# Performance work log

Measured on AMD Instinct MI355X. Metric: run time of the kernel, lower is better.

Reference implementation:

```python
import jax, jax.numpy as jnp
import numpy as np

EMB_DIM = 1024
NHEAD = 16
HEAD_DIM = EMB_DIM // NHEAD
SLEN = 1024
BSZ = 8
NEG_INF = -1e30


def setup_inputs() -> dict:
    key = jax.random.key(0)
    ks = jax.random.split(key, 8)
    q = jax.random.normal(ks[0], (SLEN, BSZ, EMB_DIM), dtype=jnp.float32)
    k = jax.random.normal(ks[1], (SLEN, BSZ, EMB_DIM), dtype=jnp.float32)
    v = jax.random.normal(ks[2], (SLEN, BSZ, EMB_DIM), dtype=jnp.float32)
    mask = jax.random.randint(ks[3], (BSZ * NHEAD, SLEN, SLEN), 0, 2).astype(jnp.bool_)
    # xavier_uniform bound for square [E,E] matrices
    bound = float(np.sqrt(6.0 / (EMB_DIM + EMB_DIM)))
    Wq = jax.random.uniform(ks[4], (EMB_DIM, EMB_DIM), jnp.float32, -bound, bound)
    Wk = jax.random.uniform(ks[5], (EMB_DIM, EMB_DIM), jnp.float32, -bound, bound)
    Wv = jax.random.uniform(ks[6], (EMB_DIM, EMB_DIM), jnp.float32, -bound, bound)
    Wo = jax.random.uniform(ks[7], (EMB_DIM, EMB_DIM), jnp.float32, -bound, bound)
    return {"q": q, "k": k, "v": v, "mask": mask, "Wq": Wq, "Wk": Wk, "Wv": Wv, "Wo": Wo}


def reference(q, k, v, mask, Wq, Wk, Wv, Wo):
    slen, bsz, emb = q.shape
    scaling = float(HEAD_DIM) ** -0.5
    # F.linear(x, W) = x @ W.T
    query = q @ Wq.T  # [slen, bsz, E]
    key_ = k @ Wk.T
    value = v @ Wv.T
    # -> [bsz*nhead, slen, head_dim]
    def split_heads(x):
        return x.reshape(slen, bsz * NHEAD, HEAD_DIM).transpose(1, 0, 2)
    query = split_heads(query)
    key_ = split_heads(key_)
    value = split_heads(value)
    attn_weight = jnp.einsum('bqd,bkd->bqk', query, key_) * scaling  # [B*H, S, S]
    attn_weight = jnp.where(mask, NEG_INF, attn_weight)
    attn_score = jax.nn.softmax(attn_weight, axis=-1)
    # attn_mask=True: post-softmax multiplicative mask
    attn_score = attn_score * (~mask).astype(attn_score.dtype)
    # dropout is identity in eval mode
    attn_output = jnp.einsum('bqk,bkd->bqd', attn_score, value)  # [B*H, S, hd]
    attn_output = attn_output.transpose(1, 0, 2).reshape(slen, bsz, emb)
    return attn_output @ Wo.T
```

## Files before the change

### kernel.cpp

```cpp
#include <hip/hip_runtime.h>


typedef __attribute__((ext_vector_type(8))) short bf16x8;
typedef __attribute__((ext_vector_type(8))) unsigned short u16x8;
typedef __attribute__((ext_vector_type(4))) float f32x4;

#define LOG2E 1.44269504088896340736f

__device__ __forceinline__ unsigned short bfbits(float f) {
  unsigned u = __builtin_bit_cast(unsigned, f);
  u += 0x7fffu + ((u >> 16) & 1u);
  return (unsigned short)(u >> 16);
}
__device__ __forceinline__ unsigned pk2(float a, float b) {
  return (unsigned)bfbits(a) | ((unsigned)bfbits(b) << 16);
}
__device__ __forceinline__ void async16(const void* src, void* dst_lds) {
  __builtin_amdgcn_global_load_lds(
      (const __attribute__((address_space(1))) unsigned int*)src,
      (__attribute__((address_space(3))) unsigned int*)dst_lds, 16, 0, 0);
}

__global__ __launch_bounds__(256) void cvt_kernel(
    const float* __restrict__ q, const float* __restrict__ k, const float* __restrict__ v,
    const float* __restrict__ wq, const float* __restrict__ wk,
    const float* __restrict__ wv, const float* __restrict__ wo,
    unsigned short* __restrict__ Xin, unsigned short* __restrict__ Wbf)
{
  const unsigned u = blockIdx.x * 256u + threadIdx.x;
  const float* src;
  unsigned short* dst;
  if (u < 3145728u) {
    const unsigned z = u >> 20, r = u & 1048575u;
    src = (z == 0 ? q : z == 1 ? k : v) + (size_t)r * 8;
    dst = Xin + (size_t)z * 8388608u + (size_t)r * 8;
  } else {
    const unsigned u2 = u - 3145728u, wz = u2 >> 17, r = u2 & 131071u;
    src = (wz == 0 ? wq : wz == 1 ? wk : wz == 2 ? wv : wo) + (size_t)r * 8;
    dst = Wbf + (size_t)wz * 1048576u + (size_t)r * 8;
  }
  f32x4 a = *(const f32x4*)src;
  f32x4 b = *(const f32x4*)(src + 4);
  u16x8 o;
  o[0]=bfbits(a[0]); o[1]=bfbits(a[1]); o[2]=bfbits(a[2]); o[3]=bfbits(a[3]);
  o[4]=bfbits(b[0]); o[5]=bfbits(b[1]); o[6]=bfbits(b[2]); o[7]=bfbits(b[3]);
  *(u16x8*)dst = o;
}

__global__ void detect_mask(const unsigned* __restrict__ m, int* __restrict__ flag)
{
  unsigned ok = 1u;
#pragma unroll 8
  for (int i = 0; i < 64; ++i) {
    unsigned w = m[(threadIdx.x << 6) + i];
    ok &= (w <= 1u) ? 1u : 0u;
  }
  unsigned long long vote = __ballot(ok != 0u);
  if (threadIdx.x == 0) *flag = (vote == ~0ull) ? 1 : 0;
}

template<int OUTF32>
__global__ __launch_bounds__(512) void gemm2ph(
    const unsigned short* __restrict__ A,
    const unsigned short* __restrict__ B,
    void* __restrict__ Cv, float scale, int M, int N, int K)
{
  const int tid = threadIdx.x;
  const int w = tid >> 6, lane = tid & 63, c = lane & 15, g = lane >> 4;
  const int wr = w >> 1, wc = w & 1;

  const int nwg = gridDim.x, cpx = nwg >> 3, bid = blockIdx.x;
  const int swz = (bid & 7) * cpx + (bid >> 3);
  const int ntx = N >> 7;
  const int bx = swz % ntx, by = swz / ntx;
  const int rowA = by * 256, rowB = bx * 128;

  __shared__ unsigned short As[2][256 * 64];
  __shared__ unsigned short Bs[2][128 * 64];

  f32x4 acc[4][4];
#pragma unroll
  for (int i = 0; i < 4; ++i)
#pragma unroll
    for (int j = 0; j < 4; ++j) acc[i][j] = (f32x4){0.f, 0.f, 0.f, 0.f};

  const int srow = tid >> 3, skc = tid & 7;
  const int wbase = (tid & ~63) * 16;

#pragma unroll
  for (int i = 0; i < 4; ++i)
    async16(A + (size_t)(rowA + i * 64 + srow) * K + skc * 8,
            (char*)&As[0][0] + i * 8192 + wbase);
#pragma unroll
  for (int j = 0; j < 2; ++j)
    async16(B + (size_t)(rowB + j * 64 + srow) * K + skc * 8,
            (char*)&Bs[0][0] + j * 8192 + wbase);
  __syncthreads();

  int buf = 0;
  const int nk = K >> 6;
  for (int kt = 0; kt < nk; ++kt) {
    if (kt + 1 < nk) {
      const int k1 = (kt + 1) << 6, bo = buf ^ 1;
#pragma unroll
      for (int i = 0; i < 4; ++i)
        async16(A + (size_t)(rowA + i * 64 + srow) * K + k1 + skc * 8,
                (char*)&As[bo][0] + i * 8192 + wbase);
#pragma unroll
      for (int j = 0; j < 2; ++j)
        async16(B + (size_t)(rowB + j * 64 + srow) * K + k1 + skc * 8,
                (char*)&Bs[bo][0] + j * 8192 + wbase);
    }
    bf16x8 af[4][2], bfr[4][2];
#pragma unroll
    for (int x = 0; x < 4; ++x)
#pragma unroll
      for (int ks = 0; ks < 2; ++ks) {
        af[x][ks]  = *(const bf16x8*)&As[buf][(wr * 64 + x * 16 + c) * 64 + ks * 32 + (g << 3)];
        bfr[x][ks] = *(const bf16x8*)&Bs[buf][(wc * 64 + x * 16 + c) * 64 + ks * 32 + (g << 3)];
      }
#pragma unroll
    for (int ks = 0; ks < 2; ++ks)
#pragma unroll
      for (int mf = 0; mf < 4; ++mf)
#pragma unroll
        for (int nf = 0; nf < 4; ++nf)
          acc[mf][nf] = __builtin_amdgcn_mfma_f32_16x16x32_bf16(af[mf][ks], bfr[nf][ks], acc[mf][nf], 0, 0, 0);
    __syncthreads();
    buf ^= 1;
  }

  const int r0 = rowA + wr * 64, c0 = rowB + wc * 64;
  if (OUTF32) {
    float* O = (float*)Cv;
#pragma unroll
    for (int mf = 0; mf < 4; ++mf)
#pragma unroll
      for (int nf = 0; nf < 4; ++nf)
#pragma unroll
        for (int j = 0; j < 4; ++j)
          O[(size_t)(r0 + mf * 16 + g * 4 + j) * N + c0 + nf * 16 + c] = acc[mf][nf][j] * scale;
  } else {
    unsigned short* O = (unsigned short*)Cv;
#pragma unroll
    for (int mf = 0; mf < 4; ++mf)
#pragma unroll
      for (int nf = 0; nf < 4; ++nf)
#pragma unroll
        for (int j = 0; j < 4; ++j)
          O[(size_t)(r0 + mf * 16 + g * 4 + j) * N + c0 + nf * 16 + c] = bfbits(acc[mf][nf][j] * scale);
  }
}

__global__ __launch_bounds__(256) void transpose_v(
    const unsigned short* __restrict__ Xp2, unsigned short* __restrict__ Vt)
{
  const int tid = threadIdx.x;
  const int bh = blockIdx.y, b = bh >> 4, h = bh & 15;
  const int s0 = blockIdx.x << 6;
  __shared__ unsigned short T[64 * 68];
#pragma unroll
  for (int p = 0; p < 2; ++p) {
    const int idx = (p << 8) + tid, sr = idx >> 3, ch2 = idx & 7;
    *(u16x8*)&T[sr * 68 + ch2 * 8] =
        *(const u16x8*)(Xp2 + ((size_t)((s0 + sr) * 8 + b) << 10) + (h << 6) + ch2 * 8);
  }
  __syncthreads();
#pragma unroll
  for (int p = 0; p < 2; ++p) {
    const int idx = (p << 8) + tid, dr = idx >> 3, ch2 = idx & 7;
    u16x8 o;
#pragma unroll
    for (int e = 0; e < 8; ++e) o[e] = T[(ch2 * 8 + e) * 68 + dr];
    *(u16x8*)(Vt + ((size_t)(bh * 64 + dr) << 10) + s0 + ch2 * 8) = o;
  }
}

__device__ __forceinline__ void load_mask4(unsigned mv[4], const void* maskp, bool mi32,
                                           size_t base, int g) {
  if (mi32) {
    const int* mrow = (const int*)maskp + base + (g << 2);
#pragma unroll
    for (int mf = 0; mf < 4; ++mf) {
      const int4 w4 = *(const int4*)(mrow + mf * 16);
      mv[mf] = (w4.x ? 1u : 0u) | (w4.y ? 0x100u : 0u) | (w4.z ? 0x10000u : 0u) | (w4.w ? 0x1000000u : 0u);
    }
  } else {
    const unsigned char* mrow = (const unsigned char*)maskp + base + (g << 2);
#pragma unroll
    for (int mf = 0; mf < 4; ++mf) mv[mf] = *(const unsigned*)(mrow + mf * 16);
  }
}

__global__ __launch_bounds__(256) void attn_kernel(
    const unsigned short* __restrict__ Qp,
    const unsigned short* __restrict__ Kp,
    const unsigned short* __restrict__ Vt,
    const void*           __restrict__ maskp,
    const int*            __restrict__ mflag,
    unsigned short* __restrict__ AO)
{
  const int tid = threadIdx.x;
  const int w = tid >> 6, lane = tid & 63, c = lane & 15, g = lane >> 4;
  const int bh = blockIdx.y, b = bh >> 4, h = bh & 15;
  const int qb0 = blockIdx.x << 6;
  const int qrow = qb0 + (w << 4) + c;
  const bool mi32 = (*mflag != 0);

  __shared__ unsigned short Ksm[64 * 72];
  __shared__ unsigned short Vsm[64 * 72];
  __shared__ unsigned short Psm[4][16 * 72];

  bf16x8 qf[2];
  {
    const unsigned short* qp = Qp + ((size_t)(qrow * 8 + b) << 10) + (h << 6) + (g << 3);
    qf[0] = *(const bf16x8*)qp;
    qf[1] = *(const bf16x8*)(qp + 32);
  }

  const int row0 = tid >> 3, ch = tid & 7;
  const unsigned short* Vg = Vt + ((size_t)bh << 16);
  const size_t mbase0 = ((size_t)bh << 20) + ((size_t)qrow << 10);

  bf16x8 kr[2], vr[2];
#pragma unroll
  for (int p = 0; p < 2; ++p) {
    const int r = row0 + p * 32;
    kr[p] = *(const bf16x8*)(Kp + ((size_t)(r * 8 + b) << 10) + (h << 6) + (ch << 3));
    vr[p] = *(const bf16x8*)(Vg + ((size_t)r << 10) + (ch << 3));
  }
  unsigned mv[4];
  load_mask4(mv, maskp, mi32, mbase0, g);

  f32x4 oacc[4];
#pragma unroll
  for (int i = 0; i < 4; ++i) oacc[i] = (f32x4){0.f, 0.f, 0.f, 0.f};
  float mrun = -1e30f, lrun = 0.f;

  for (int t = 0; t < 16; ++t) {
    const int kk0 = t << 6;
    __syncthreads();
#pragma unroll
    for (int p = 0; p < 2; ++p) {
      const int r = row0 + p * 32;
      *(bf16x8*)&Ksm[r * 72 + (ch << 3)] = kr[p];
      *(bf16x8*)&Vsm[r * 72 + (ch << 3)] = vr[p];
    }
    __syncthreads();
    unsigned mvN[4];
    if (t < 15) {
      const int kk1 = kk0 + 64;
#pragma unroll
      for (int p = 0; p < 2; ++p) {
        const int r = row0 + p * 32;
        kr[p] = *(const bf16x8*)(Kp + ((size_t)((kk1 + r) * 8 + b) << 10) + (h << 6) + (ch << 3));
        vr[p] = *(const bf16x8*)(Vg + ((size_t)r << 10) + kk1 + (ch << 3));
      }
      load_mask4(mvN, maskp, mi32, mbase0 + kk1, g);
    }
    f32x4 sacc[4];
#pragma unroll
    for (int i = 0; i < 4; ++i) sacc[i] = (f32x4){0.f, 0.f, 0.f, 0.f};
#pragma unroll
    for (int d2 = 0; d2 < 2; ++d2) {
#pragma unroll
      for (int mf = 0; mf < 4; ++mf) {
        bf16x8 kf = *(const bf16x8*)&Ksm[(mf * 16 + c) * 72 + d2 * 32 + (g << 3)];
        sacc[mf] = __builtin_amdgcn_mfma_f32_16x16x32_bf16(kf, qf[d2], sacc[mf], 0, 0, 0);
      }
    }
    float tmax = -1e30f;
#pragma unroll
    for (int mf = 0; mf < 4; ++mf)
#pragma unroll
      for (int j = 0; j < 4; ++j) {
        float s = sacc[mf][j];
        if ((mv[mf] >> (8 * j)) & 0xffu) s = -1e30f;
        sacc[mf][j] = s;
        tmax = fmaxf(tmax, s);
      }
    tmax = fmaxf(tmax, __shfl_xor(tmax, 16));
    tmax = fmaxf(tmax, __shfl_xor(tmax, 32));
    const float mnew = fmaxf(mrun, tmax);
    const float alpha = __builtin_amdgcn_exp2f((mrun - mnew) * LOG2E);
    float tsum = 0.f;
    float pv[4][4];
#pragma unroll
    for (int mf = 0; mf < 4; ++mf)
#pragma unroll
      for (int j = 0; j < 4; ++j) {
        const float p = __builtin_amdgcn_exp2f((sacc[mf][j] - mnew) * LOG2E);
        pv[mf][j] = p;
        tsum += p;
      }
    tsum += __shfl_xor(tsum, 16);
    tsum += __shfl_xor(tsum, 32);
    lrun = lrun * alpha + tsum;
    mrun = mnew;
#pragma unroll
    for (int i = 0; i < 4; ++i) {
      oacc[i][0] *= alpha; oacc[i][1] *= alpha; oacc[i][2] *= alpha; oacc[i][3] *= alpha;
    }
#pragma unroll
    for (int mf = 0; mf < 4; ++mf) {
      uint2 t2;
      t2.x = pk2(pv[mf][0], pv[mf][1]);
      t2.y = pk2(pv[mf][2], pv[mf][3]);
      *(uint2*)&Psm[w][c * 72 + mf * 16 + (g << 2)] = t2;
    }
#pragma unroll
    for (int ks = 0; ks < 2; ++ks) {
      bf16x8 pf = *(const bf16x8*)&Psm[w][c * 72 + ks * 32 + (g << 3)];
#pragma unroll
      for (int mf = 0; mf < 4; ++mf) {
        bf16x8 vf = *(const bf16x8*)&Vsm[(mf * 16 + c) * 72 + ks * 32 + (g << 3)];
        oacc[mf] = __builtin_amdgcn_mfma_f32_16x16x32_bf16(vf, pf, oacc[mf], 0, 0, 0);
      }
    }
    if (t < 15) {
      mv[0] = mvN[0]; mv[1] = mvN[1]; mv[2] = mvN[2]; mv[3] = mvN[3];
    }
  }
  const float inv = 1.0f / lrun;
#pragma unroll
  for (int mf = 0; mf < 4; ++mf) {
    uint2 t2;
    t2.x = pk2(oacc[mf][0] * inv, oacc[mf][1] * inv);
    t2.y = pk2(oacc[mf][2] * inv, oacc[mf][3] * inv);
    *(uint2*)(AO + ((size_t)(qrow * 8 + b) << 10) + (h << 6) + mf * 16 + (g << 2)) = t2;
  }
}

extern "C" void kernel_launch(void* const* d_in, const int* in_sizes, int n_in,
                              void* d_out, int out_size, void* d_ws, size_t ws_size,
                              hipStream_t stream)
{
  const float* q  = (const float*)d_in[0];
  const float* k  = (const float*)d_in[1];
  const float* v  = (const float*)d_in[2];
  const void*  mask = (const void*)d_in[3];
  const float* wq = (const float*)d_in[4];
  const float* wk = (const float*)d_in[5];
  const float* wv = (const float*)d_in[6];
  const float* wo = (const float*)d_in[7];

  unsigned short* ws  = (unsigned short*)d_ws;
  unsigned short* Xin = ws;
  unsigned short* Wbf = ws + 25165824u;
  unsigned short* Xp  = ws + 29360128u;
  unsigned short* Vt  = ws + 8388608u;
  unsigned short* AO  = ws;
  int* mfl            = (int*)(ws + 16777216u);

  cvt_kernel<<<14336, 256, 0, stream>>>(q, k, v, wq, wk, wv, wo, Xin, Wbf);
  gemm2ph<0><<<256, 512, 0, stream>>>(Xin,             Wbf,            Xp,             0.125f, 8192, 1024, 1024);
  gemm2ph<0><<<256, 512, 0, stream>>>(Xin + 8388608u,  Wbf + 1048576u, Xp + 8388608u,  1.0f,   8192, 1024, 1024);
  gemm2ph<0><<<256, 512, 0, stream>>>(Xin + 16777216u, Wbf + 2097152u, Xp + 16777216u, 1.0f,   8192, 1024, 1024);
  detect_mask<<<1, 64, 0, stream>>>((const unsigned*)mask, mfl);
  transpose_v<<<dim3(16, 128), 256, 0, stream>>>(Xp + 16777216u, Vt);
  attn_kernel<<<dim3(16, 128), 256, 0, stream>>>(Xp, Xp + 8388608u, Vt, mask, mfl, AO);
  gemm2ph<1><<<256, 512, 0, stream>>>(AO, Wbf + 3145728u, d_out, 1.0f, 8192, 1024, 1024);
}
```

Before: 311.6 us.

## Pack boolean mask into bitmask inside projection GEMMs and read bits in attention

The three QKV projection GEMM launches now also convert the byte or int mask into a packed 1-bit-per-element buffer, each block handling a slice across its first k-iterations. The attention kernel then reads 64-bit words of mask bits per tile instead of bytes, which cuts mask traffic in the bandwidth-heavy attention pass. The cost is an extra full read of the mask overlapped with GEMM compute, some added GEMM work, and a hardcoded 256-block swizzle. The bf16 conversion store is also reworked to pack pairs of values into 32-bit words.

Result: slower. 346.7 us (+11.2%).

```diff
diff --git a/kernel.cpp b/kernel.cpp
--- a/kernel.cpp
+++ b/kernel.cpp
@@ -19,6 +19,25 @@
   __builtin_amdgcn_global_load_lds(
       (const __attribute__((address_space(1))) unsigned int*)src,
       (__attribute__((address_space(3))) unsigned int*)dst_lds, 16, 0, 0);
+}
+__device__ __forceinline__ unsigned nz4i(uint4 w) {
+  return (w.x ? 1u : 0u) | (w.y ? 2u : 0u) | (w.z ? 4u : 0u) | (w.w ? 8u : 0u);
+}
+__device__ __forceinline__ unsigned nz4b(unsigned w) {
+  return ((w & 0xFFu) ? 1u : 0u) | ((w & 0xFF00u) ? 2u : 0u) |
+         ((w & 0xFF0000u) ? 4u : 0u) | ((w & 0xFF000000u) ? 8u : 0u);
+}
+
+__global__ void detect_mask(const unsigned* __restrict__ m, int* __restrict__ flag)
+{
+  unsigned ok = 1u;
+#pragma unroll 8
+  for (int i = 0; i < 64; ++i) {
+    unsigned w = m[(threadIdx.x << 6) + i];
+    ok &= (w <= 1u) ? 1u : 0u;
+  }
+  unsigned long long vote = __ballot(ok != 0u);
+  if (threadIdx.x == 0) *flag = (vote == ~0ull) ? 1 : 0;
 }
 
 __global__ __launch_bounds__(256) void cvt_kernel(
@@ -41,42 +60,37 @@
   }
   f32x4 a = *(const f32x4*)src;
   f32x4 b = *(const f32x4*)(src + 4);
-  u16x8 o;
-  o[0]=bfbits(a[0]); o[1]=bfbits(a[1]); o[2]=bfbits(a[2]); o[3]=bfbits(a[3]);
-  o[4]=bfbits(b[0]); o[5]=bfbits(b[1]); o[6]=bfbits(b[2]); o[7]=bfbits(b[3]);
-  *(u16x8*)dst = o;
-}
-
-__global__ void detect_mask(const unsigned* __restrict__ m, int* __restrict__ flag)
-{
-  unsigned ok = 1u;
-#pragma unroll 8
-  for (int i = 0; i < 64; ++i) {
-    unsigned w = m[(threadIdx.x << 6) + i];
-    ok &= (w <= 1u) ? 1u : 0u;
-  }
-  unsigned long long vote = __ballot(ok != 0u);
-  if (threadIdx.x == 0) *flag = (vote == ~0ull) ? 1 : 0;
+  uint4 o;
+  o.x = pk2(a[0], a[1]); o.y = pk2(a[2], a[3]);
+  o.z = pk2(b[0], b[1]); o.w = pk2(b[2], b[3]);
+  *(uint4*)dst = o;
 }
 
 template<int OUTF32>
 __global__ __launch_bounds__(512) void gemm2ph(
     const unsigned short* __restrict__ A,
     const unsigned short* __restrict__ B,
-    void* __restrict__ Cv, float scale, int M, int N, int K)
+    void* __restrict__ Cv, float scale, int M, int N, int K,
+    const void* __restrict__ maskp, const int* __restrict__ mflag,
+    unsigned* __restrict__ Mp32, unsigned packLo, unsigned packHi)
 {
   const int tid = threadIdx.x;
   const int w = tid >> 6, lane = tid & 63, c = lane & 15, g = lane >> 4;
   const int wr = w >> 1, wc = w & 1;
 
-  const int nwg = gridDim.x, cpx = nwg >> 3, bid = blockIdx.x;
-  const int swz = (bid & 7) * cpx + (bid >> 3);
+  const int bid = blockIdx.x;
+  const int swz = (bid & 7) * 32 + (bid >> 3);
   const int ntx = N >> 7;
   const int bx = swz % ntx, by = swz / ntx;
   const int rowA = by * 256, rowB = bx * 128;
 
   __shared__ unsigned short As[2][256 * 64];
   __shared__ unsigned short Bs[2][128 * 64];
+
+  const bool doPack = packHi > packLo;
+  const unsigned slice0 = packLo + (unsigned)bid * 5462u;
+  const unsigned slice1 = doPack ? (packHi < slice0 + 5462u ? packHi : slice0 + 5462u) : 0u;
+  const bool mi32 = doPack && (*mflag != 0);
 
   f32x4 acc[4][4];
 #pragma unroll
@@ -111,6 +125,28 @@
         async16(B + (size_t)(rowB + j * 64 + srow) * K + k1 + skc * 8,
                 (char*)&Bs[bo][0] + j * 8192 + wbase);
     }
+    if (doPack && kt < 11) {
+      const unsigned u = slice0 + (unsigned)kt * 512u + tid;
+      if (u < slice1) {
+        unsigned bits = 0u;
+        if (mi32) {
+          const uint4* s = (const uint4*)((const int*)maskp + (size_t)u * 32);
+#pragma unroll
+          for (int hh = 0; hh < 2; ++hh) {
+            const uint4 w0 = s[hh * 4 + 0], w1 = s[hh * 4 + 1];
+            const uint4 w2 = s[hh * 4 + 2], w3 = s[hh * 4 + 3];
+            const unsigned b16 = nz4i(w0) | (nz4i(w1) << 4) | (nz4i(w2) << 8) | (nz4i(w3) << 12);
+            bits |= b16 << (hh * 16);
+          }
+        } else {
+          const uint4* s = (const uint4*)((const unsigned char*)maskp + (size_t)u * 32);
+          const uint4 w0 = s[0], w1 = s[1];
+          bits = nz4b(w0.x) | (nz4b(w0.y) << 4) | (nz4b(w0.z) << 8) | (nz4b(w0.w) << 12) |
+                 (nz4b(w1.x) << 16) | (nz4b(w1.y) << 20) | (nz4b(w1.z) << 24) | (nz4b(w1.w) << 28);
+        }
+        Mp32[u] = bits;
+      }
+    }
     bf16x8 af[4][2], bfr[4][2];
 #pragma unroll
     for (int x = 0; x < 4; ++x)
@@ -176,28 +212,11 @@
   }
 }
 
-__device__ __forceinline__ void load_mask4(unsigned mv[4], const void* maskp, bool mi32,
-                                           size_t base, int g) {
-  if (mi32) {
-    const int* mrow = (const int*)maskp + base + (g << 2);
-#pragma unroll
-    for (int mf = 0; mf < 4; ++mf) {
-      const int4 w4 = *(const int4*)(mrow + mf * 16);
-      mv[mf] = (w4.x ? 1u : 0u) | (w4.y ? 0x100u : 0u) | (w4.z ? 0x10000u : 0u) | (w4.w ? 0x1000000u : 0u);
-    }
-  } else {
-    const unsigned char* mrow = (const unsigned char*)maskp + base + (g << 2);
-#pragma unroll
-    for (int mf = 0; mf < 4; ++mf) mv[mf] = *(const unsigned*)(mrow + mf * 16);
-  }
-}
-
 __global__ __launch_bounds__(256) void attn_kernel(
     const unsigned short* __restrict__ Qp,
     const unsigned short* __restrict__ Kp,
     const unsigned short* __restrict__ Vt,
-    const void*           __restrict__ maskp,
-    const int*            __restrict__ mflag,
+    const unsigned long long* __restrict__ Mp,
     unsigned short* __restrict__ AO)
 {
   const int tid = threadIdx.x;
@@ -205,7 +224,6 @@
   const int bh = blockIdx.y, b = bh >> 4, h = bh & 15;
   const int qb0 = blockIdx.x << 6;
   const int qrow = qb0 + (w << 4) + c;
-  const bool mi32 = (*mflag != 0);
 
   __shared__ unsigned short Ksm[64 * 72];
   __shared__ unsigned short Vsm[64 * 72];
@@ -220,7 +238,7 @@
 
   const int row0 = tid >> 3, ch = tid & 7;
   const unsigned short* Vg = Vt + ((size_t)bh << 16);
-  const size_t mbase0 = ((size_t)bh << 20) + ((size_t)qrow << 10);
+  const unsigned long long* Mrow = Mp + (((size_t)bh << 10) + qrow) * 16;
 
   bf16x8 kr[2], vr[2];
 #pragma unroll
@@ -229,8 +247,7 @@
     kr[p] = *(const bf16x8*)(Kp + ((size_t)(r * 8 + b) << 10) + (h << 6) + (ch << 3));
     vr[p] = *(const bf16x8*)(Vg + ((size_t)r << 10) + (ch << 3));
   }
-  unsigned mv[4];
-  load_mask4(mv, maskp, mi32, mbase0, g);
+  unsigned long long mw = Mrow[0];
 
   f32x4 oacc[4];
 #pragma unroll
@@ -247,7 +264,7 @@
       *(bf16x8*)&Vsm[r * 72 + (ch << 3)] = vr[p];
     }
     __syncthreads();
-    unsigned mvN[4];
+    unsigned long long mwN = 0ull;
     if (t < 15) {
       const int kk1 = kk0 + 64;
 #pragma unroll
@@ -256,7 +273,7 @@
         kr[p] = *(const bf16x8*)(Kp + ((size_t)((kk1 + r) * 8 + b) << 10) + (h << 6) + (ch << 3));
         vr[p] = *(const bf16x8*)(Vg + ((size_t)r << 10) + kk1 + (ch << 3));
       }
-      load_mask4(mvN, maskp, mi32, mbase0 + kk1, g);
+      mwN = Mrow[t + 1];
     }
     f32x4 sacc[4];
 #pragma unroll
@@ -271,14 +288,16 @@
     }
     float tmax = -1e30f;
 #pragma unroll
-    for (int mf = 0; mf < 4; ++mf)
+    for (int mf = 0; mf < 4; ++mf) {
+      const unsigned nib = ((unsigned)(mw >> (mf * 16 + (g << 2)))) & 0xFu;
 #pragma unroll
       for (int j = 0; j < 4; ++j) {
         float s = sacc[mf][j];
-        if ((mv[mf] >> (8 * j)) & 0xffu) s = -1e30f;
+        if ((nib >> j) & 1u) s = -1e30f;
         sacc[mf][j] = s;
         tmax = fmaxf(tmax, s);
       }
+    }
     tmax = fmaxf(tmax, __shfl_xor(tmax, 16));
     tmax = fmaxf(tmax, __shfl_xor(tmax, 32));
     const float mnew = fmaxf(mrun, tmax);
@@ -317,9 +336,7 @@
         oacc[mf] = __builtin_amdgcn_mfma_f32_16x16x32_bf16(vf, pf, oacc[mf], 0, 0, 0);
       }
     }
-    if (t < 15) {
-      mv[0] = mvN[0]; mv[1] = mvN[1]; mv[2] = mvN[2]; mv[3] = mvN[3];
-    }
+    mw = mwN;
   }
   const float inv = 1.0f / lrun;
 #pragma unroll
@@ -348,16 +365,24 @@
   unsigned short* Xin = ws;
   unsigned short* Wbf = ws + 25165824u;
   unsigned short* Xp  = ws + 29360128u;
+  unsigned* Mp32      = (unsigned*)(ws + 54525952u);
+  int* mfl            = (int*)(ws + 62914560u);
   unsigned short* Vt  = ws + 8388608u;
   unsigned short* AO  = ws;
-  int* mfl            = (int*)(ws + 16777216u);
-
+
+  const unsigned PT = 4194304u;
+  const unsigned p1 = 1398102u, p2 = 2796203u;
+
+  detect_mask<<<1, 64, 0, stream>>>((const unsigned*)mask, mfl);
   cvt_kernel<<<14336, 256, 0, stream>>>(q, k, v, wq, wk, wv, wo, Xin, Wbf);
-  gemm2ph<0><<<256, 512, 0, stream>>>(Xin,             Wbf,            Xp,             0.125f, 8192, 1024, 1024);
-  gemm2ph<0><<<256, 512, 0, stream>>>(Xin + 8388608u,  Wbf + 1048576u, Xp + 8388608u,  1.0f,   8192, 1024, 1024);
-  gemm2ph<0><<<256, 512, 0, stream>>>(Xin + 16777216u, Wbf + 2097152u, Xp + 16777216u, 1.0f,   8192, 1024, 1024);
-  detect_mask<<<1, 64, 0, stream>>>((const unsigned*)mask, mfl);
+  gemm2ph<0><<<256, 512, 0, stream>>>(Xin,             Wbf,            Xp,             0.125f, 8192, 1024, 1024,
+                                      mask, mfl, Mp32, 0u, p1);
+  gemm2ph<0><<<256, 512, 0, stream>>>(Xin + 8388608u,  Wbf + 1048576u, Xp + 8388608u,  1.0f,   8192, 1024, 1024,
+                                      mask, mfl, Mp32, p1, p2);
+  gemm2ph<0><<<256, 512, 0, stream>>>(Xin + 16777216u, Wbf + 2097152u, Xp + 16777216u, 1.0f,   8192, 1024, 1024,
+                                      mask, mfl, Mp32, p2, PT);
   transpose_v<<<dim3(16, 128), 256, 0, stream>>>(Xp + 16777216u, Vt);
-  attn_kernel<<<dim3(16, 128), 256, 0, stream>>>(Xp, Xp + 8388608u, Vt, mask, mfl, AO);
-  gemm2ph<1><<<256, 512, 0, stream>>>(AO, Wbf + 3145728u, d_out, 1.0f, 8192, 1024, 1024);
-}
+  attn_kernel<<<dim3(16, 128), 256, 0, stream>>>(Xp, Xp + 8388608u, Vt, (const unsigned long long*)Mp32, AO);
+  gemm2ph<1><<<256, 512, 0, stream>>>(AO, Wbf + 3145728u, d_out, 1.0f, 8192, 1024, 1024,
+                                      mask, mfl, Mp32, 0u, 0u);
+}
```
